# Optimization experiments

Measured on AMD Instinct MI355X. Metric: run time of the kernel, lower is better.

## Reference

```python
import jax, jax.numpy as jnp
import numpy as np

NDIM = 7  # window side; N = 49
NUM_HEADS = 12

def _rel_pos_index(ndim=NDIM):
    coords = np.stack(np.meshgrid(np.arange(ndim), np.arange(ndim), indexing='ij'))  # [2,7,7]
    cf = coords.reshape(2, -1)                      # [2,49]
    rel = cf[:, :, None] - cf[:, None, :]           # [2,49,49]
    rel = rel.transpose(1, 2, 0).copy()             # [49,49,2]
    rel[:, :, 0] += ndim - 1
    rel[:, :, 1] += ndim - 1
    rel[:, :, 0] *= 2 * ndim - 1
    return jnp.asarray(rel.sum(-1), dtype=jnp.int32)  # [49,49]

def setup_inputs() -> dict:
    key = jax.random.key(0)
    ks = jax.random.split(key, 6)
    B, N, C = 1024, NDIM * NDIM, 768
    x = jax.random.normal(ks[0], (B, N, C), dtype=jnp.float32)
    prev = jax.random.normal(ks[1], (B, NUM_HEADS, N, N), dtype=jnp.float32)
    # weights stored as [in, out] so forward is x @ W (matches torch Linear math)
    qkv_w = jax.random.normal(ks[2], (C, 3 * C), dtype=jnp.float32) * 0.02
    proj_w = jax.random.normal(ks[3], (C, C), dtype=jnp.float32) * 0.02
    proj_b = jax.random.normal(ks[4], (C,), dtype=jnp.float32) * 0.02
    bias_table = jax.random.normal(ks[5], ((2 * NDIM - 1) ** 2, NUM_HEADS), dtype=jnp.float32) * 0.02
    rel_idx = _rel_pos_index()
    return {"x": x, "prev": prev, "qkv_w": qkv_w, "proj_w": proj_w,
            "proj_b": proj_b, "bias_table": bias_table, "rel_idx": rel_idx}

def reference(x, prev, qkv_w, proj_w, proj_b, bias_table, rel_idx):
    B, N, C = x.shape
    H = NUM_HEADS
    hd = C // H
    scale = hd ** -0.5
    qkv = (x @ qkv_w).reshape(B, N, 3, H, hd)
    q = qkv[:, :, 0].transpose(0, 2, 1, 3)  # [B,H,N,hd]
    k = qkv[:, :, 1].transpose(0, 2, 1, 3)
    v = qkv[:, :, 2].transpose(0, 2, 1, 3)
    attn_score = jnp.einsum('bhnd,bhmd->bhnm', q, k) * scale  # [B,H,N,N]
    bias = bias_table[rel_idx.reshape(-1)].reshape(N, N, H).transpose(2, 0, 1)  # [H,N,N]
    attn_score = attn_score + bias[None]
    attn_score = attn_score + prev          # res_score=True path
    prev_out = attn_score
    attn = jax.nn.softmax(attn_score, axis=-1)
    out = jnp.einsum('bhnm,bhmd->bhnd', attn, v).transpose(0, 2, 1, 3).reshape(B, N, C)
    out = out @ proj_w + proj_b
    return (out, prev_out)
```

## Files before the change

kernel.cpp:

```cpp
#include <hip/hip_runtime.h>

typedef unsigned short u16;
typedef unsigned int u32;
typedef float f32x4 __attribute__((ext_vector_type(4)));
typedef __bf16 bf16x8 __attribute__((ext_vector_type(8)));

#define DEV static __device__ __forceinline__

DEV u16 f2bf(float f) {
  u32 u = __builtin_bit_cast(u32, f);
  u += 0x7fffu + ((u >> 16) & 1u);
  return (u16)(u >> 16);
}

DEV float bf2f(u16 v) {
  u32 u = ((u32)v) << 16;
  return __builtin_bit_cast(float, u);
}

DEV void gload_lds16(const void* g, void* l) {
  __builtin_amdgcn_global_load_lds(
      (const __attribute__((address_space(1))) u32*)g,
      (__attribute__((address_space(3))) u32*)l, 16, 0, 0);
}


__global__ __launch_bounds__(256) void cvt_bf16(const float* __restrict__ in,
                                                u16* __restrict__ out, int n4) {
  int i = blockIdx.x * 256 + threadIdx.x;
  const int stride = gridDim.x * 256;
  for (; i < n4; i += stride) {
    const float4 v = ((const float4*)in)[i];
    ushort4 o;
    o.x = f2bf(v.x); o.y = f2bf(v.y); o.z = f2bf(v.z); o.w = f2bf(v.w);
    ((ushort4*)out)[i] = o;
  }
}

__global__ __launch_bounds__(256) void cvtT_tile(const float* __restrict__ in,
                                                 u16* __restrict__ out, int K, int N) {
  __shared__ float tile[32][33];
  const int nbx = N >> 5;
  const int bx = blockIdx.x % nbx, by = blockIdx.x / nbx;
  const int tx = threadIdx.x & 31, ty = threadIdx.x >> 5;
  const int gcol = bx * 32 + tx;
#pragma unroll
  for (int j = 0; j < 4; ++j) {
    const int r = ty + 8 * j;
    tile[r][tx] = in[(long)(by * 32 + r) * N + gcol];
  }
  __syncthreads();
#pragma unroll
  for (int j = 0; j < 4; ++j) {
    const int r = ty + 8 * j;
    out[(long)(bx * 32 + r) * K + by * 32 + tx] = f2bf(tile[tx][r]);
  }
}

__global__ __launch_bounds__(256) void bias_pre(const float* __restrict__ bias_table,
                                                const int* __restrict__ rel_idx,
                                                float* __restrict__ biasM) {
  int i = blockIdx.x * 256 + threadIdx.x;
  if (i >= 12 * 2401) return;
  int h = i / 2401, p = i - h * 2401;
  biasM[i] = bias_table[rel_idx[p] * 12 + h];
}

template <bool OUT_BF16>
__global__ __launch_bounds__(512, 2) void gemm256(
    const u16* __restrict__ A, const u16* __restrict__ BT,
    void* __restrict__ C, const float* __restrict__ bias,
    int M, int N, int K, int nbn) {
  __shared__ alignas(16) char lds[163840];
  const int t = threadIdx.x;
  const int w = t >> 6, l = t & 63, lr = l & 15, lhi = l >> 4;
  const int wr = w >> 2, wc = w & 3;

  const int nwg = gridDim.x;
  const int q = nwg >> 3, r = nwg & 7;
  const int xcd = blockIdx.x & 7, lid = blockIdx.x >> 3;
  const int swz = (xcd < r ? xcd * (q + 1) : r * (q + 1) + (xcd - r) * q) + lid;
  const int bm = swz / nbn, bn = swz % nbn;

  const int T = K >> 5;
  const long Kb = (long)K * 2;

  const int unswz = (l & 7) ^ (l >> 3);
  const int arow = 2 * (l >> 3) + (unswz >> 2);
  const int acolb = (unswz & 3) << 4;
  const char* gA0 = (const char*)A + (long)(bm * 256 + w * 32 + arow) * Kb + acolb;
  const char* gA1 = gA0 + 16 * Kb;
  const char* gB0 = (const char*)BT + (long)(bn * 256 + w * 32 + arow) * Kb + acolb;
  const char* gB1 = gB0 + 16 * Kb;
  const int ldA0 = w * 2048, ldA1 = w * 2048 + 1024;
  const int ldB0 = 16384 + w * 2048, ldB1 = 16384 + w * 2048 + 1024;

#define STAGE(tt, bb)                           \
  {                                             \
    const long ko = (long)(tt) * 64;            \
    gload_lds16(gA0 + ko, lds + (bb) + ldA0);   \
    gload_lds16(gA1 + ko, lds + (bb) + ldA1);   \
    gload_lds16(gB0 + ko, lds + (bb) + ldB0);   \
    gload_lds16(gB1 + ko, lds + (bb) + ldB1);   \
  }
#define BAR                                  \
  asm volatile("" ::: "memory");             \
  __builtin_amdgcn_s_barrier();              \
  asm volatile("" ::: "memory")

  const int rblk = ((((lr & 1) << 2) | lhi) ^ (lr >> 1));
  const int aoff0 = (wr * 64 + (lr >> 1)) * 128 + rblk * 16;
  const int boff0 = 16384 + (wc * 32 + (lr >> 1)) * 128 + rblk * 16;

  f32x4 acc[8][4];
#pragma unroll
  for (int m = 0; m < 8; ++m)
#pragma unroll
    for (int n = 0; n < 4; ++n) acc[m][n] = (f32x4){0.f, 0.f, 0.f, 0.f};
  bf16x8 afrX[4], bfrX[4], afrY[4], bfrY[4];

#define CLUSTER1(S)                                                        \
  __builtin_amdgcn_s_setprio(1);                                           \
  _Pragma("unroll") for (int m = 0; m < 4; ++m)                            \
      _Pragma("unroll") for (int n = 0; n < 4; ++n)                        \
          acc[m][n] = __builtin_amdgcn_mfma_f32_16x16x32_bf16(             \
              afr##S[m], bfr##S[n], acc[m][n], 0, 0, 0);                   \
  __builtin_amdgcn_s_setprio(0)
#define CLUSTER2(S)                                                        \
  __builtin_amdgcn_s_setprio(1);                                           \
  _Pragma("unroll") for (int m = 0; m < 4; ++m)                            \
      _Pragma("unroll") for (int n = 0; n < 4; ++n)                        \
          acc[m + 4][n] = __builtin_amdgcn_mfma_f32_16x16x32_bf16(         \
              afr2[m], bfr##S[n], acc[m + 4][n], 0, 0, 0);                 \
  __builtin_amdgcn_s_setprio(0)

#define BODY(kt, S, R)                                                     \
  {                                                                        \
    int sbb = bb0 - 32768; if (sbb < 0) sbb = 131072;       \
    int nbb = bb0 + 32768; if (nbb > 131072) nbb = 0;       \
    if ((kt) + 4 < T) STAGE((kt) + 4, sbb);                                \
    bf16x8 afr2[4];                                                        \
    _Pragma("unroll") for (int m = 0; m < 4; ++m)                          \
        afr2[m] = *(const bf16x8*)(lds + bb0 + aoff0 + (m + 4) * 1024);    \
    CLUSTER1(S);                                                           \
    const int rb = ((kt) + 1 < T) ? nbb : bb0;                             \
    _Pragma("unroll") for (int n = 0; n < 4; ++n)                          \
        bfr##R[n] = *(const bf16x8*)(lds + rb + boff0 + n * 1024);         \
    CLUSTER2(S);                                                           \
    _Pragma("unroll") for (int m = 0; m < 4; ++m)                          \
        afr##R[m] = *(const bf16x8*)(lds + rb + aoff0 + m * 1024);         \
    if ((kt) + 4 < T) {                                                    \
      asm volatile("s_waitcnt vmcnt(8)" ::: "memory");                     \
    } else if ((kt) + 3 < T) {                                             \
      asm volatile("s_waitcnt vmcnt(4)" ::: "memory");                     \
    } else {                                                               \
      asm volatile("s_waitcnt vmcnt(0)" ::: "memory");                     \
    }                                                                      \
    BAR;                                                                   \
    bb0 = nbb;                                                             \
  }

  STAGE(0, 0); STAGE(1, 32768); STAGE(2, 65536); STAGE(3, 98304);
  asm volatile("s_waitcnt vmcnt(8)" ::: "memory");
  BAR;
  int bb0 = 0;
#pragma unroll
  for (int n = 0; n < 4; ++n) bfrX[n] = *(const bf16x8*)(lds + boff0 + n * 1024);
#pragma unroll
  for (int m = 0; m < 4; ++m) afrX[m] = *(const bf16x8*)(lds + aoff0 + m * 1024);

  for (int i = 0; i < T / 2; ++i) {
    BODY(2 * i, X, Y);
    BODY(2 * i + 1, Y, X);
  }
#undef STAGE
#undef BAR
#undef CLUSTER1
#undef CLUSTER2
#undef BODY

  const int row0 = bm * 256 + wr * 128 + 4 * lhi;
  const int col0 = bn * 256 + wc * 64 + lr;
  if (OUT_BF16) {
    u16* Cc = (u16*)C;
#pragma unroll
    for (int m = 0; m < 8; ++m)
#pragma unroll
      for (int rr = 0; rr < 4; ++rr) {
        const long row = row0 + m * 16 + rr;
#pragma unroll
        for (int n = 0; n < 4; ++n)
          Cc[row * N + col0 + n * 16] = f2bf(acc[m][n][rr]);
      }
  } else {
    float* Cf = (float*)C;
    float bv[4];
#pragma unroll
    for (int n = 0; n < 4; ++n) bv[n] = bias[col0 + n * 16];
#pragma unroll
    for (int m = 0; m < 8; ++m)
#pragma unroll
      for (int rr = 0; rr < 4; ++rr) {
        const long row = row0 + m * 16 + rr;
#pragma unroll
        for (int n = 0; n < 4; ++n)
          Cf[row * N + col0 + n * 16] = acc[m][n][rr] + bv[n];
      }
  }
}

__global__ __launch_bounds__(256) void attn_kernel(
    const u16* __restrict__ qkv,
    const float* __restrict__ prev,
    const float* __restrict__ biasM,
    float* __restrict__ prev_out,
    u16* __restrict__ attn_out) {
  __shared__ u16 Qs[64][72];
  __shared__ u16 Ks[64][72];
  __shared__ u16 VTs[64][72];
  __shared__ u16 SB[2432];

  const int bh = blockIdx.x;
  const int b = bh / 12, h = bh % 12;
  const int t = threadIdx.x, w = t >> 6, l = t & 63, lr = l & 15, lhi = l >> 4;

  const u16* base = qkv + (long)(b * 49) * 2304 + h * 64;
  for (int idx = t; idx < 49 * 16; idx += 256) {
    const int n = idx >> 4, c4 = (idx & 15) << 2;
    const u16* rp = base + (long)n * 2304;
    ushort4 qv = *(const ushort4*)(rp + c4);
    ushort4 kv = *(const ushort4*)(rp + 768 + c4);
    ushort4 vv = *(const ushort4*)(rp + 1536 + c4);
    *(ushort4*)&Qs[n][c4] = qv;
    *(ushort4*)&Ks[n][c4] = kv;
    VTs[c4 + 0][n] = vv.x;
    VTs[c4 + 1][n] = vv.y;
    VTs[c4 + 2][n] = vv.z;
    VTs[c4 + 3][n] = vv.w;
  }
  for (int idx = t; idx < 1024; idx += 256) {
    const int j = idx & 15;
    if (j) VTs[idx >> 4][48 + j] = 0;
  }

  float prevR[10], biasR[10];
  {
    const float* pv = prev + (long)bh * 2401;
    const float* bm = biasM + h * 2401;
#pragma unroll
    for (int k = 0; k < 10; ++k) {
      const int i = t + 256 * k;
      if (i < 2401) {
        prevR[k] = pv[i];
        biasR[k] = bm[i];
      }
    }
  }

  asm volatile("s_waitcnt lgkmcnt(0)" ::: "memory");
  __builtin_amdgcn_s_barrier();
  asm volatile("" ::: "memory");

  bf16x8 af0 = *(const bf16x8*)&Qs[16 * w + lr][lhi * 8];
  bf16x8 af1 = *(const bf16x8*)&Qs[16 * w + lr][32 + lhi * 8];
  f32x4 sacc[4];
#pragma unroll
  for (int tc = 0; tc < 4; ++tc) {
    sacc[tc] = (f32x4){0.f, 0.f, 0.f, 0.f};
    bf16x8 b0 = *(const bf16x8*)&Ks[16 * tc + lr][lhi * 8];
    bf16x8 b1 = *(const bf16x8*)&Ks[16 * tc + lr][32 + lhi * 8];
    sacc[tc] = __builtin_amdgcn_mfma_f32_16x16x32_bf16(af0, b0, sacc[tc], 0, 0, 0);
    sacc[tc] = __builtin_amdgcn_mfma_f32_16x16x32_bf16(af1, b1, sacc[tc], 0, 0, 0);
  }

  asm volatile("s_waitcnt vmcnt(0)" ::: "memory");
#pragma unroll
  for (int k = 0; k < 10; ++k) {
    const int i = t + 256 * k;
    if (i < 2401) SB[i] = f2bf(prevR[k] + biasR[k]);
  }
  asm volatile("s_waitcnt lgkmcnt(0)" ::: "memory");
  __builtin_amdgcn_s_barrier();
  asm volatile("" ::: "memory");

  u16 (*Ps)[72] = Qs;
  const int nrow0 = 16 * w + 4 * lhi;
  float rs[4];
#pragma unroll
  for (int r = 0; r < 4; ++r) {
    const int row = nrow0 + r;
    const bool rv = row < 49;
    float sv[4];
#pragma unroll
    for (int tc = 0; tc < 4; ++tc) {
      const int col = 16 * tc + lr;
      const bool valid = rv && (col < 49);
      const int sidx = (row < 49 ? row : 48) * 49 + (col < 49 ? col : 48);
      const float pb = bf2f(SB[sidx]);
      const float s = sacc[tc][r] * 0.125f + pb;
      if (valid) SB[sidx] = f2bf(s);
      sv[tc] = valid ? s : -INFINITY;
    }
    float mx = fmaxf(fmaxf(sv[0], sv[1]), fmaxf(sv[2], sv[3]));
#pragma unroll
    for (int off = 8; off; off >>= 1) mx = fmaxf(mx, __shfl_xor(mx, off, 16));
    float e[4], sum = 0.f;
#pragma unroll
    for (int tc = 0; tc < 4; ++tc) {
      e[tc] = __expf(sv[tc] - mx);
      sum += e[tc];
    }
#pragma unroll
    for (int off = 8; off; off >>= 1) sum += __shfl_xor(sum, off, 16);
    rs[r] = 1.0f / sum;
#pragma unroll
    for (int tc = 0; tc < 4; ++tc)
      Ps[row][16 * tc + lr] = rv ? f2bf(e[tc]) : (u16)0;
  }
  __syncthreads();

  bf16x8 pf0 = *(const bf16x8*)&Ps[16 * w + lr][lhi * 8];
  bf16x8 pf1 = *(const bf16x8*)&Ps[16 * w + lr][32 + lhi * 8];
  f32x4 oacc[4];
#pragma unroll
  for (int dc = 0; dc < 4; ++dc) {
    oacc[dc] = (f32x4){0.f, 0.f, 0.f, 0.f};
    bf16x8 v0 = *(const bf16x8*)&VTs[16 * dc + lr][lhi * 8];
    bf16x8 v1 = *(const bf16x8*)&VTs[16 * dc + lr][32 + lhi * 8];
    oacc[dc] = __builtin_amdgcn_mfma_f32_16x16x32_bf16(pf0, v0, oacc[dc], 0, 0, 0);
    oacc[dc] = __builtin_amdgcn_mfma_f32_16x16x32_bf16(pf1, v1, oacc[dc], 0, 0, 0);
  }

#pragma unroll
  for (int r = 0; r < 4; ++r) {
    const int row = nrow0 + r;
    if (row < 49) {
#pragma unroll
      for (int dc = 0; dc < 4; ++dc)
        Ks[row][16 * dc + lr] = f2bf(oacc[dc][r] * rs[r]);
    }
  }
  __syncthreads();

  {
    u16* ob = attn_out + (long)(b * 49) * 768 + h * 64;
    for (int idx = t; idx < 49 * 8; idx += 256) {
      const int row = idx >> 3, cc = (idx & 7) << 3;
      *(ulonglong2*)&ob[(long)row * 768 + cc] = *(const ulonglong2*)&Ks[row][cc];
    }
    float* pout = prev_out + (long)bh * 2401;
    for (int i = t; i < 2401; i += 256) pout[i] = bf2f(SB[i]);
  }
}

extern "C" void kernel_launch(void* const* d_in, const int* in_sizes, int n_in,
                              void* d_out, int out_size, void* d_ws, size_t ws_size,
                              hipStream_t stream) {
  const float* x = (const float*)d_in[0];
  const float* prev = (const float*)d_in[1];
  const float* qkv_w = (const float*)d_in[2];
  const float* proj_w = (const float*)d_in[3];
  const float* proj_b = (const float*)d_in[4];
  const float* bias_table = (const float*)d_in[5];
  const int* rel_idx = (const int*)d_in[6];

  const int B = in_sizes[0] / (49 * 768);
  const int M = B * 49;

  float* out0 = (float*)d_out;
  float* out1 = out0 + (size_t)M * 768;

  char* ws = (char*)d_ws;
  u16* xbf = (u16*)ws;
  u16* qkvbf = (u16*)(ws + (size_t)M * 768 * 2);
  u16* qkvwT = (u16*)(ws + (size_t)M * 768 * 2 + (size_t)M * 2304 * 2);
  u16* projwT = qkvwT + 2304 * 768;
  float* biasM = (float*)(projwT + 768 * 768);

  bias_pre<<<(12 * 2401 + 255) / 256, 256, 0, stream>>>(bias_table, rel_idx, biasM);
  cvt_bf16<<<2048, 256, 0, stream>>>(x, xbf, M * 768 / 4);
  cvtT_tile<<<(2304 / 32) * (768 / 32), 256, 0, stream>>>(qkv_w, qkvwT, 768, 2304);
  cvtT_tile<<<(768 / 32) * (768 / 32), 256, 0, stream>>>(proj_w, projwT, 768, 768);

  gemm256<true><<<(M / 256) * (2304 / 256), 512, 0, stream>>>(
      xbf, qkvwT, qkvbf, nullptr, M, 2304, 768, 2304 / 256);

  attn_kernel<<<B * 12, 256, 0, stream>>>(qkvbf, prev, biasM, out1, xbf);

  gemm256<false><<<(M / 256) * (768 / 256), 512, 0, stream>>>(
      xbf, projwT, out0, proj_b, M, 768, 768, 768 / 256);
}
```

Baseline: 471.1 us.

## Restructure bf16 GEMM main loop to BK=64 double-buffered ping-pong schedule

The 256x256 GEMM mainloop moves from a 4-stage ring of BK=32 tiles to two 64 KB buffers of BK=64 tiles. The A and B halves are loaded in staggered quarter-stages interleaved between four MFMA clusters, with explicit barriers and lgkmcnt waits, in the style of a ping-pong schedule. LDS drops from 160 KB to 128 KB and the swizzle changes to an XOR over 8 columns. The aim is better overlap of global-to-LDS loads with MFMA work and fewer barrier phases per unit of K, at the cost of many more barriers per iteration and tighter vmcnt accounting.

```diff
diff --git a/kernel.cpp b/kernel.cpp
--- a/kernel.cpp
+++ b/kernel.cpp
@@ -71,7 +71,7 @@
     const u16* __restrict__ A, const u16* __restrict__ BT,
     void* __restrict__ C, const float* __restrict__ bias,
     int M, int N, int K, int nbn) {
-  __shared__ alignas(16) char lds[163840];
+  __shared__ alignas(16) char lds[131072];
   const int t = threadIdx.x;
   const int w = t >> 6, l = t & 63, lr = l & 15, lhi = l >> 4;
   const int wr = w >> 2, wc = w & 3;
@@ -82,102 +82,113 @@
   const int swz = (xcd < r ? xcd * (q + 1) : r * (q + 1) + (xcd - r) * q) + lid;
   const int bm = swz / nbn, bn = swz % nbn;
 
-  const int T = K >> 5;
+  const int T = K >> 6;
   const long Kb = (long)K * 2;
 
-  const int unswz = (l & 7) ^ (l >> 3);
-  const int arow = 2 * (l >> 3) + (unswz >> 2);
-  const int acolb = (unswz & 3) << 4;
-  const char* gA0 = (const char*)A + (long)(bm * 256 + w * 32 + arow) * Kb + acolb;
-  const char* gA1 = gA0 + 16 * Kb;
-  const char* gB0 = (const char*)BT + (long)(bn * 256 + w * 32 + arow) * Kb + acolb;
-  const char* gB1 = gB0 + 16 * Kb;
-  const int ldA0 = w * 2048, ldA1 = w * 2048 + 1024;
-  const int ldB0 = 16384 + w * 2048, ldB1 = 16384 + w * 2048 + 1024;
-
-#define STAGE(tt, bb)                           \
-  {                                             \
-    const long ko = (long)(tt) * 64;            \
-    gload_lds16(gA0 + ko, lds + (bb) + ldA0);   \
-    gload_lds16(gA1 + ko, lds + (bb) + ldA1);   \
-    gload_lds16(gB0 + ko, lds + (bb) + ldB0);   \
-    gload_lds16(gB1 + ko, lds + (bb) + ldB1);   \
-  }
+  const int srow = w * 16 + (l >> 3);
+  const int sb = (l & 7) ^ ((l >> 3) & 7);
+  const char* gAs = (const char*)A + (long)(bm * 256 + srow) * Kb + sb * 16;
+  const char* gBs = (const char*)BT + (long)(bn * 256 + srow) * Kb + sb * 16;
+  const int ldw = w * 2048;
+
+#define SA0(tt) { const int bb=((tt)&1)*65536; const long ko=(long)(tt)*128;      \
+  gload_lds16(gAs+ko, lds+bb+ldw); gload_lds16(gAs+8*Kb+ko, lds+bb+ldw+1024); }
+#define SA1(tt) { const int bb=((tt)&1)*65536; const long ko=(long)(tt)*128;      \
+  gload_lds16(gAs+128*Kb+ko, lds+bb+16384+ldw);                                   \
+  gload_lds16(gAs+136*Kb+ko, lds+bb+16384+ldw+1024); }
+#define SB0(tt) { const int bb=((tt)&1)*65536; const long ko=(long)(tt)*128;      \
+  gload_lds16(gBs+ko, lds+bb+32768+ldw); gload_lds16(gBs+8*Kb+ko, lds+bb+32768+ldw+1024); }
+#define SB1(tt) { const int bb=((tt)&1)*65536; const long ko=(long)(tt)*128;      \
+  gload_lds16(gBs+128*Kb+ko, lds+bb+49152+ldw);                                   \
+  gload_lds16(gBs+136*Kb+ko, lds+bb+49152+ldw+1024); }
 #define BAR                                  \
   asm volatile("" ::: "memory");             \
   __builtin_amdgcn_s_barrier();              \
   asm volatile("" ::: "memory")
-
-  const int rblk = ((((lr & 1) << 2) | lhi) ^ (lr >> 1));
-  const int aoff0 = (wr * 64 + (lr >> 1)) * 128 + rblk * 16;
-  const int boff0 = 16384 + (wc * 32 + (lr >> 1)) * 128 + rblk * 16;
+#define LGKM0                                              \
+  asm volatile("s_waitcnt lgkmcnt(0)" ::: "memory");       \
+  __builtin_amdgcn_sched_barrier(0)
+#define MFMA16(AM, AN, AS, BS)                                               \
+  __builtin_amdgcn_s_setprio(1);                                             \
+  _Pragma("unroll") for (int mt = 0; mt < 4; ++mt)                           \
+  _Pragma("unroll") for (int nt = 0; nt < 2; ++nt) {                         \
+    acc[mt + AM][nt + AN] = __builtin_amdgcn_mfma_f32_16x16x32_bf16(         \
+        AS[mt][0], BS[nt][0], acc[mt + AM][nt + AN], 0, 0, 0);               \
+    acc[mt + AM][nt + AN] = __builtin_amdgcn_mfma_f32_16x16x32_bf16(         \
+        AS[mt][1], BS[nt][1], acc[mt + AM][nt + AN], 0, 0, 0);               \
+  }                                                                          \
+  __builtin_amdgcn_s_setprio(0)
+
+  const int aoffL = (wr * 128 + lr) * 128 + ((lhi ^ (lr & 7)) << 4);
+  const int boffL = 32768 + (wc * 64 + lr) * 128 + ((lhi ^ (lr & 7)) << 4);
 
   f32x4 acc[8][4];
 #pragma unroll
   for (int m = 0; m < 8; ++m)
 #pragma unroll
     for (int n = 0; n < 4; ++n) acc[m][n] = (f32x4){0.f, 0.f, 0.f, 0.f};
-  bf16x8 afrX[4], bfrX[4], afrY[4], bfrY[4];
-
-#define CLUSTER1(S)                                                        \
-  __builtin_amdgcn_s_setprio(1);                                           \
-  _Pragma("unroll") for (int m = 0; m < 4; ++m)                            \
-      _Pragma("unroll") for (int n = 0; n < 4; ++n)                        \
-          acc[m][n] = __builtin_amdgcn_mfma_f32_16x16x32_bf16(             \
-              afr##S[m], bfr##S[n], acc[m][n], 0, 0, 0);                   \
-  __builtin_amdgcn_s_setprio(0)
-#define CLUSTER2(S)                                                        \
-  __builtin_amdgcn_s_setprio(1);                                           \
-  _Pragma("unroll") for (int m = 0; m < 4; ++m)                            \
-      _Pragma("unroll") for (int n = 0; n < 4; ++n)                        \
-          acc[m + 4][n] = __builtin_amdgcn_mfma_f32_16x16x32_bf16(         \
-              afr2[m], bfr##S[n], acc[m + 4][n], 0, 0, 0);                 \
-  __builtin_amdgcn_s_setprio(0)
-
-#define BODY(kt, S, R)                                                     \
-  {                                                                        \
-    int sbb = bb0 - 32768; if (sbb < 0) sbb = 131072;       \
-    int nbb = bb0 + 32768; if (nbb > 131072) nbb = 0;       \
-    if ((kt) + 4 < T) STAGE((kt) + 4, sbb);                                \
-    bf16x8 afr2[4];                                                        \
-    _Pragma("unroll") for (int m = 0; m < 4; ++m)                          \
-        afr2[m] = *(const bf16x8*)(lds + bb0 + aoff0 + (m + 4) * 1024);    \
-    CLUSTER1(S);                                                           \
-    const int rb = ((kt) + 1 < T) ? nbb : bb0;                             \
-    _Pragma("unroll") for (int n = 0; n < 4; ++n)                          \
-        bfr##R[n] = *(const bf16x8*)(lds + rb + boff0 + n * 1024);         \
-    CLUSTER2(S);                                                           \
-    _Pragma("unroll") for (int m = 0; m < 4; ++m)                          \
-        afr##R[m] = *(const bf16x8*)(lds + rb + aoff0 + m * 1024);         \
-    if ((kt) + 4 < T) {                                                    \
-      asm volatile("s_waitcnt vmcnt(8)" ::: "memory");                     \
-    } else if ((kt) + 3 < T) {                                             \
-      asm volatile("s_waitcnt vmcnt(4)" ::: "memory");                     \
-    } else {                                                               \
-      asm volatile("s_waitcnt vmcnt(0)" ::: "memory");                     \
-    }                                                                      \
-    BAR;                                                                   \
-    bb0 = nbb;                                                             \
-  }
-
-  STAGE(0, 0); STAGE(1, 32768); STAGE(2, 65536); STAGE(3, 98304);
-  asm volatile("s_waitcnt vmcnt(8)" ::: "memory");
+
+  SA0(0); SB0(0); SB1(0); SA1(0);
+  SB0(1); SB1(1); SA0(1);
+  asm volatile("s_waitcnt vmcnt(6)" ::: "memory");
   BAR;
-  int bb0 = 0;
-#pragma unroll
-  for (int n = 0; n < 4; ++n) bfrX[n] = *(const bf16x8*)(lds + boff0 + n * 1024);
-#pragma unroll
-  for (int m = 0; m < 4; ++m) afrX[m] = *(const bf16x8*)(lds + aoff0 + m * 1024);
-
-  for (int i = 0; i < T / 2; ++i) {
-    BODY(2 * i, X, Y);
-    BODY(2 * i + 1, Y, X);
-  }
-#undef STAGE
+
+  for (int kt = 0; kt < T; ++kt) {
+    const int bb = (kt & 1) * 65536;
+    bf16x8 aC[4][2], b0[2][2], b1[2][2];
+#pragma unroll
+    for (int mt = 0; mt < 4; ++mt) {
+      aC[mt][0] = *(const bf16x8*)(lds + (bb + aoffL + mt * 2048));
+      aC[mt][1] = *(const bf16x8*)(lds + ((bb + aoffL + mt * 2048) ^ 64));
+    }
+#pragma unroll
+    for (int nt = 0; nt < 2; ++nt) {
+      b0[nt][0] = *(const bf16x8*)(lds + (bb + boffL + nt * 2048));
+      b0[nt][1] = *(const bf16x8*)(lds + ((bb + boffL + nt * 2048) ^ 64));
+    }
+    if (kt + 1 < T) SA1(kt + 1);
+    asm volatile("s_waitcnt lgkmcnt(8)" ::: "memory");
+    BAR;
+    LGKM0;
+    MFMA16(0, 0, aC, b0);
+    BAR;
+#pragma unroll
+    for (int nt = 0; nt < 2; ++nt) {
+      b1[nt][0] = *(const bf16x8*)(lds + (bb + boffL + (nt + 2) * 2048));
+      b1[nt][1] = *(const bf16x8*)(lds + ((bb + boffL + (nt + 2) * 2048) ^ 64));
+    }
+    BAR;
+    LGKM0;
+    MFMA16(0, 2, aC, b1);
+    BAR;
+#pragma unroll
+    for (int mt = 0; mt < 4; ++mt) {
+      aC[mt][0] = *(const bf16x8*)(lds + (bb + aoffL + (mt + 4) * 2048));
+      aC[mt][1] = *(const bf16x8*)(lds + ((bb + aoffL + (mt + 4) * 2048) ^ 64));
+    }
+    if (kt + 2 < T) SB0(kt + 2);
+    BAR;
+    LGKM0;
+    MFMA16(4, 2, aC, b1);
+    BAR;
+    if (kt + 2 < T) { SB1(kt + 2); SA0(kt + 2); }
+    BAR;
+    LGKM0;
+    MFMA16(4, 0, aC, b0);
+    if (kt + 3 <= T) {
+      asm volatile("s_waitcnt vmcnt(6)" ::: "memory");
+    } else {
+      asm volatile("s_waitcnt vmcnt(0)" ::: "memory");
+    }
+    BAR;
+  }
+#undef SA0
+#undef SA1
+#undef SB0
+#undef SB1
 #undef BAR
-#undef CLUSTER1
-#undef CLUSTER2
-#undef BODY
+#undef LGKM0
+#undef MFMA16
 
   const int row0 = bm * 256 + wr * 128 + 4 * lhi;
   const int col0 = bn * 256 + wc * 64 + lr;
```

Measured after the change: 468.1 us. Within noise of the previous version (-0.6%).
